# Performance work log

Hardware: AMD Instinct MI355X
Metric: run time of the kernel (lower is better)

The kernel has to match this reference:

```python
import jax, jax.numpy as jnp
import numpy as np

KH, KW = 5, 5               # kernel_size from init_kwargs
PAD_H, PAD_W = (KH - 1) // 2, (KW - 1) // 2
MED_IDX = (KH * KW - 1) // 2  # torch.median -> lower median; exact middle for odd counts


def setup_inputs() -> dict:
    key = jax.random.key(0)
    x = jax.random.normal(key, (2, 4, 1024, 1024), dtype=jnp.float32)  # B,C,H,W
    return {"x": x}


def reference(x):
    # Zero-pad spatially, matching F.conv2d(padding=(k-1)//2), stride=1.
    B, C, H, W = x.shape
    xp = jnp.pad(x, ((0, 0), (0, 0), (PAD_H, PAD_H), (PAD_W, PAD_W)))
    # Extract K*K shifted views (equivalent to the binary grouped conv2d),
    # stacked into [B, C, KH*KW, H, W] — same layout as features.view(b,c,-1,h,w).
    patches = jnp.stack(
        [xp[:, :, i:i + H, j:j + W] for i in range(KH) for j in range(KW)],
        axis=2,
    )
    # torch.median(dim=2)[0]: sort the window axis and take the middle element.
    return jnp.sort(patches, axis=2)[:, :, MED_IDX]
```

## Files before the change

kernel.cpp:

```cpp
#include <hip/hip_runtime.h>

#define IMG_W 1024
#define IMG_H 1024

typedef _Float16 h2 __attribute__((ext_vector_type(2)));

__device__ __forceinline__ h2 mn(h2 a, h2 b) {
    h2 r; asm("v_pk_min_f16 %0, %1, %2" : "=v"(r) : "v"(a), "v"(b)); return r;
}
__device__ __forceinline__ h2 mx(h2 a, h2 b) {
    h2 r; asm("v_pk_max_f16 %0, %1, %2" : "=v"(r) : "v"(a), "v"(b)); return r;
}
__device__ __forceinline__ void ce(h2 &a, h2 &b) { h2 t = mn(a, b); b = mx(a, b); a = t; }
__device__ __forceinline__ h2 med3p(h2 a, h2 b, h2 c) {
    return mx(mn(a, b), mn(mx(a, b), c));
}
__device__ __forceinline__ void sort5(h2 &a0, h2 &a1, h2 &a2, h2 &a3, h2 &a4) {
    ce(a0, a1); ce(a3, a4); ce(a2, a4); ce(a2, a3);
    ce(a0, a3); ce(a0, a2); ce(a1, a4); ce(a1, a3); ce(a1, a2);
}
__device__ __forceinline__ void sort4(h2 &a, h2 &b, h2 &c, h2 &d) {
    ce(a, b); ce(c, d); ce(a, c); ce(b, d); ce(b, c);
}

__device__ __forceinline__ h2 bch2(unsigned u) { return __builtin_bit_cast(h2, u); }

struct Row { h2 a, b, c, d, e; };
struct Raw { unsigned d0, d1, d2; };

#define LDS_DW 35
#define LDS_PAD 2560

__device__ __forceinline__ Raw load_raw(const unsigned* __restrict__ ldsf, int row, int tx) {
    const unsigned* p = ldsf + row * LDS_DW + tx;
    Raw r; r.d0 = p[0]; r.d1 = p[1]; r.d2 = p[2];
    return r;
}
__device__ __forceinline__ Row sort_row(Raw r) {
    h2 p0 = bch2(r.d0);
    h2 p1 = bch2((r.d0 >> 16) | (r.d1 << 16));
    h2 p2 = bch2(r.d1);
    h2 p3 = bch2((r.d1 >> 16) | (r.d2 << 16));
    h2 p4 = bch2(r.d2);
    sort5(p0, p1, p2, p3, p4);
    return {p0, p1, p2, p3, p4};
}

__device__ __forceinline__ h2 tail13(h2 A, h2 B, h2 c1a, h2 c1b, h2 c1c,
                                     h2 c2a, h2 c2b, h2 c2c,
                                     h2 c3a, h2 c3b, h2 c3c, h2 D, h2 E) {
    ce(A, D); ce(c1a, c3a); ce(A, c1a);
    ce(B, E); ce(c1b, c3b); ce(E, c3b);
    h2 e0 = B, e1 = D, e2 = E, e3 = c1a, e4 = c1b, e5 = c3a, e6 = c1c;
    ce(e0, e1); ce(e2, e3); ce(e4, e5);
    ce(e0, e2); ce(e4, e6); ce(e0, e4);
    ce(e1, e3); ce(e5, e6); ce(e3, e6);
    h2 f0 = e1, f1 = e2, f2 = e3, f3 = e4, f4 = e5, f5 = c2a;
    ce(f0, f1); ce(f2, f3); ce(f4, f5);
    ce(f0, f2); ce(f0, f4);
    ce(f1, f3); ce(f3, f5);
    h2 g0 = f1, g1 = f2, g2 = f3, g3 = f4, g4 = c2b;
    ce(g0, g1); ce(g2, g3);
    ce(g0, g2); ce(g0, g4);
    ce(g1, g3); ce(g3, g4);
    h2 h0 = g1, h1 = g2, h2_ = g3, h3 = c2c;
    ce(h0, h1); ce(h2_, h3); ce(h0, h2_); ce(h1, h3);
    return med3p(h1, h2_, c3c);
}

__device__ __forceinline__ void pair_medians(const Row &rb, const Row &rc, const Row &rd,
                                             const Row &re, const Row &ra, const Row &rf,
                                             h2 &out_lo, h2 &out_hi) {
    h2 s0, s1, s2, s3;
    s0 = rb.a; s1 = rc.a; s2 = rd.a; s3 = re.a; sort4(s0, s1, s2, s3);
    h2 Bl = mx(s3, ra.a), Al = mx(s2, mn(s3, ra.a));
    h2 Bh = mx(s3, rf.a), Ah = mx(s2, mn(s3, rf.a));
    s0 = rb.b; s1 = rc.b; s2 = rd.b; s3 = re.b; sort4(s0, s1, s2, s3);
    h2 c1al = s2, c1bl = s3, c1cl = mx(s1, ra.b);
    h2 c1ah = s2, c1bh = s3, c1ch = mx(s1, rf.b);
    s0 = rb.c; s1 = rc.c; s2 = rd.c; s3 = re.c; sort4(s0, s1, s2, s3);
    h2 c2al = s1, c2bl = s2, c2cl = med3p(s0, ra.c, s3);
    h2 c2ah = s1, c2bh = s2, c2ch = med3p(s0, rf.c, s3);
    s0 = rb.d; s1 = rc.d; s2 = rd.d; s3 = re.d; sort4(s0, s1, s2, s3);
    h2 c3al = s0, c3bl = s1, c3cl = mn(s2, ra.d);
    h2 c3ah = s0, c3bh = s1, c3ch = mn(s2, rf.d);
    s0 = rb.e; s1 = rc.e; s2 = rd.e; s3 = re.e; sort4(s0, s1, s2, s3);
    h2 Dl = mn(s0, ra.e), El = mn(s1, mx(s0, ra.e));
    h2 Dh = mn(s0, rf.e), Eh = mn(s1, mx(s0, rf.e));

    out_lo = tail13(Al, Bl, c1al, c1bl, c1cl, c2al, c2bl, c2cl, c3al, c3bl, c3cl, Dl, El);
    out_hi = tail13(Ah, Bh, c1ah, c1bh, c1ch, c2ah, c2bh, c2ch, c3ah, c3bh, c3ch, Dh, Eh);
}

__global__ __launch_bounds__(256, 4) void median5x5_kernel(const float* __restrict__ x,
                                                           float* __restrict__ out) {
    __shared__ unsigned ldsf[LDS_PAD];

    const int tx = threadIdx.x;
    const int ty = threadIdx.y;
    const int tid = ty * 32 + tx;
    const int plane = blockIdx.z;
    const float* src = x + (size_t)plane * IMG_H * IMG_W;

    const int gx0 = blockIdx.x * 64 - 2;
    const int gy0 = blockIdx.y * 64 - 2;

    float2 v[10];
    int oka[10], okb[10];
    #pragma unroll
    for (int k = 0; k < 10; ++k) {
        int idx = tid + k * 256;
        int r = idx / LDS_DW;
        int dc = idx - r * LDS_DW;
        int gy = gy0 + r;
        int gxa = gx0 + 2 * dc;
        int cgy = min(max(gy, 0), IMG_H - 1);
        int cgx = min(max(gxa, 0), IMG_W - 2);
        v[k] = *reinterpret_cast<const float2*>(src + (size_t)cgy * IMG_W + cgx);
        oka[k] = ((unsigned)gy < IMG_H) & ((unsigned)gxa < IMG_W);
        okb[k] = ((unsigned)gy < IMG_H) & ((unsigned)(gxa + 1) < IMG_W);
    }
    #pragma unroll
    for (int k = 0; k < 10; ++k) {
        int idx = tid + k * 256;
        float a = oka[k] ? v[k].x : 0.0f;
        float b = okb[k] ? v[k].y : 0.0f;
        ldsf[idx] = __builtin_bit_cast(unsigned, __builtin_amdgcn_cvt_pkrtz(a, b));
    }
    __syncthreads();

    const int base = ty * 8;
    Raw r0 = load_raw(ldsf, base + 0, tx), r1 = load_raw(ldsf, base + 1, tx),
        r2 = load_raw(ldsf, base + 2, tx), r3 = load_raw(ldsf, base + 3, tx),
        r4 = load_raw(ldsf, base + 4, tx), r5 = load_raw(ldsf, base + 5, tx);
    Row S0 = sort_row(r0), S1 = sort_row(r1), S2 = sort_row(r2),
        S3 = sort_row(r3), S4 = sort_row(r4), S5 = sort_row(r5);

    float* dst = out + (size_t)plane * IMG_H * IMG_W
               + (size_t)(blockIdx.y * 64 + base) * IMG_W + blockIdx.x * 64 + 2 * tx;
    h2 mlo, mhi;

#define EMIT(vv, m) do {                                                       \
        float2 o; o.x = (float)(m).x; o.y = (float)(m).y;                      \
        *reinterpret_cast<float2*>(dst + (size_t)(vv) * IMG_W) = o;            \
    } while (0)

    Raw n0 = load_raw(ldsf, base + 6, tx), n1 = load_raw(ldsf, base + 7, tx);
    pair_medians(S1, S2, S3, S4, S0, S5, mlo, mhi);
    EMIT(0, mlo); EMIT(1, mhi);
    S0 = sort_row(n0); S1 = sort_row(n1);

    n0 = load_raw(ldsf, base + 8, tx); n1 = load_raw(ldsf, base + 9, tx);
    pair_medians(S3, S4, S5, S0, S2, S1, mlo, mhi);
    EMIT(2, mlo); EMIT(3, mhi);
    S2 = sort_row(n0); S3 = sort_row(n1);

    n0 = load_raw(ldsf, base + 10, tx); n1 = load_raw(ldsf, base + 11, tx);
    pair_medians(S5, S0, S1, S2, S4, S3, mlo, mhi);
    EMIT(4, mlo); EMIT(5, mhi);
    S4 = sort_row(n0); S5 = sort_row(n1);

    pair_medians(S1, S2, S3, S4, S0, S5, mlo, mhi);
    EMIT(6, mlo); EMIT(7, mhi);
#undef EMIT
}

extern "C" void kernel_launch(void* const* d_in, const int* in_sizes, int n_in,
                              void* d_out, int out_size, void* d_ws, size_t ws_size,
                              hipStream_t stream) {
    const float* x = (const float*)d_in[0];
    float* out = (float*)d_out;
    const int planes = in_sizes[0] / (IMG_H * IMG_W);
    dim3 grid(IMG_W / 64, IMG_H / 64, planes);
    dim3 block(32, 8);
    median5x5_kernel<<<grid, block, 0, stream>>>(x, out);
}
```

Baseline: 90.30 us.

## Process two vertical tiles per block with double-buffered LDS prefetch

Each block now handles two 64x64 output tiles stacked vertically. The global loads for the second tile are issued before the first tile is computed, so their latency hides behind the sorting work, and the staged data goes into a second LDS buffer. This halves the grid and doubles LDS per block. It also keeps 30 extra registers live across the compute phase, which may lower occupancy or cause spills under the 256x4 launch bounds.

```diff
diff --git a/kernel.cpp b/kernel.cpp
--- a/kernel.cpp
+++ b/kernel.cpp
@@ -92,21 +92,13 @@
     out_hi = tail13(Ah, Bh, c1ah, c1bh, c1ch, c2ah, c2bh, c2ch, c3ah, c3bh, c3ch, Dh, Eh);
 }
 
-__global__ __launch_bounds__(256, 4) void median5x5_kernel(const float* __restrict__ x,
-                                                           float* __restrict__ out) {
-    __shared__ unsigned ldsf[LDS_PAD];
-
-    const int tx = threadIdx.x;
-    const int ty = threadIdx.y;
-    const int tid = ty * 32 + tx;
-    const int plane = blockIdx.z;
-    const float* src = x + (size_t)plane * IMG_H * IMG_W;
-
-    const int gx0 = blockIdx.x * 64 - 2;
-    const int gy0 = blockIdx.y * 64 - 2;
-
+struct Stage {
     float2 v[10];
     int oka[10], okb[10];
+};
+
+__device__ __forceinline__ void stage_issue(const float* __restrict__ src,
+                                            int gx0, int gy0, int tid, Stage &st) {
     #pragma unroll
     for (int k = 0; k < 10; ++k) {
         int idx = tid + k * 256;
@@ -116,28 +108,30 @@
         int gxa = gx0 + 2 * dc;
         int cgy = min(max(gy, 0), IMG_H - 1);
         int cgx = min(max(gxa, 0), IMG_W - 2);
-        v[k] = *reinterpret_cast<const float2*>(src + (size_t)cgy * IMG_W + cgx);
-        oka[k] = ((unsigned)gy < IMG_H) & ((unsigned)gxa < IMG_W);
-        okb[k] = ((unsigned)gy < IMG_H) & ((unsigned)(gxa + 1) < IMG_W);
+        st.v[k] = *reinterpret_cast<const float2*>(src + (size_t)cgy * IMG_W + cgx);
+        st.oka[k] = ((unsigned)gy < IMG_H) & ((unsigned)gxa < IMG_W);
+        st.okb[k] = ((unsigned)gy < IMG_H) & ((unsigned)(gxa + 1) < IMG_W);
     }
+}
+
+__device__ __forceinline__ void stage_write(unsigned* __restrict__ buf,
+                                            int tid, const Stage &st) {
     #pragma unroll
     for (int k = 0; k < 10; ++k) {
         int idx = tid + k * 256;
-        float a = oka[k] ? v[k].x : 0.0f;
-        float b = okb[k] ? v[k].y : 0.0f;
-        ldsf[idx] = __builtin_bit_cast(unsigned, __builtin_amdgcn_cvt_pkrtz(a, b));
+        float a = st.oka[k] ? st.v[k].x : 0.0f;
+        float b = st.okb[k] ? st.v[k].y : 0.0f;
+        buf[idx] = __builtin_bit_cast(unsigned, __builtin_amdgcn_cvt_pkrtz(a, b));
     }
-    __syncthreads();
-
-    const int base = ty * 8;
+}
+
+__device__ __forceinline__ void compute_tile(const unsigned* __restrict__ ldsf,
+                                             int base, int tx, float* __restrict__ dst) {
     Raw r0 = load_raw(ldsf, base + 0, tx), r1 = load_raw(ldsf, base + 1, tx),
         r2 = load_raw(ldsf, base + 2, tx), r3 = load_raw(ldsf, base + 3, tx),
         r4 = load_raw(ldsf, base + 4, tx), r5 = load_raw(ldsf, base + 5, tx);
     Row S0 = sort_row(r0), S1 = sort_row(r1), S2 = sort_row(r2),
         S3 = sort_row(r3), S4 = sort_row(r4), S5 = sort_row(r5);
-
-    float* dst = out + (size_t)plane * IMG_H * IMG_W
-               + (size_t)(blockIdx.y * 64 + base) * IMG_W + blockIdx.x * 64 + 2 * tx;
     h2 mlo, mhi;
 
 #define EMIT(vv, m) do {                                                       \
@@ -163,6 +157,35 @@
     pair_medians(S1, S2, S3, S4, S0, S5, mlo, mhi);
     EMIT(6, mlo); EMIT(7, mhi);
 #undef EMIT
+}
+
+__global__ __launch_bounds__(256, 4) void median5x5_kernel(const float* __restrict__ x,
+                                                           float* __restrict__ out) {
+    __shared__ unsigned ldsf[2][LDS_PAD];
+
+    const int tx = threadIdx.x;
+    const int ty = threadIdx.y;
+    const int tid = ty * 32 + tx;
+    const int plane = blockIdx.z;
+    const float* src = x + (size_t)plane * IMG_H * IMG_W;
+
+    const int gx0 = blockIdx.x * 64 - 2;
+    const int ty0 = blockIdx.y * 128;
+    const int base = ty * 8;
+
+    float* dst0 = out + (size_t)plane * IMG_H * IMG_W
+                + (size_t)(ty0 + base) * IMG_W + blockIdx.x * 64 + 2 * tx;
+    float* dst1 = dst0 + (size_t)64 * IMG_W;
+
+    Stage s0, s1;
+    stage_issue(src, gx0, ty0 - 2, tid, s0);
+    stage_write(ldsf[0], tid, s0);
+    __syncthreads();
+    stage_issue(src, gx0, ty0 + 62, tid, s1);
+    compute_tile(ldsf[0], base, tx, dst0);
+    stage_write(ldsf[1], tid, s1);
+    __syncthreads();
+    compute_tile(ldsf[1], base, tx, dst1);
 }
 
 extern "C" void kernel_launch(void* const* d_in, const int* in_sizes, int n_in,
@@ -171,7 +194,7 @@
     const float* x = (const float*)d_in[0];
     float* out = (float*)d_out;
     const int planes = in_sizes[0] / (IMG_H * IMG_W);
-    dim3 grid(IMG_W / 64, IMG_H / 64, planes);
+    dim3 grid(IMG_W / 64, IMG_H / 128, planes);
     dim3 block(32, 8);
     median5x5_kernel<<<grid, block, 0, stream>>>(x, out);
 }
```

Measured after the change: 90.67 us. About the same (+0.4%).

## Load interior tiles directly into LDS as fp32 via global_load_lds

Applied to the files above, without the earlier changes.

Interior blocks now copy their 68x72 fp32 halo tile straight from global memory into LDS with 16-byte global_load_lds, bypassing registers. The fp16 packing moves to read time, converting each window pair with cvt_pkrtz. Border blocks keep a clamped, zero-padded float2 path. The LDS tile doubles in size because it is stored as fp32, the occupancy hint rises to 6, and the inline-asm min/max become builtins. The aim is fewer VGPRs and instructions in the staging phase, at the cost of more LDS traffic and extra conversions in the compute loop.

```diff
diff --git a/kernel.cpp b/kernel.cpp
--- a/kernel.cpp
+++ b/kernel.cpp
@@ -2,18 +2,21 @@
 
 #define IMG_W 1024
 #define IMG_H 1024
+#define ROW_F 72
+#define LDS_F 5120
 
 typedef _Float16 h2 __attribute__((ext_vector_type(2)));
+typedef __attribute__((address_space(3))) unsigned lds_u32_t;
+typedef const __attribute__((address_space(1))) unsigned glb_u32_t;
 
-__device__ __forceinline__ h2 mn(h2 a, h2 b) {
-    h2 r; asm("v_pk_min_f16 %0, %1, %2" : "=v"(r) : "v"(a), "v"(b)); return r;
-}
-__device__ __forceinline__ h2 mx(h2 a, h2 b) {
-    h2 r; asm("v_pk_max_f16 %0, %1, %2" : "=v"(r) : "v"(a), "v"(b)); return r;
-}
+__device__ __forceinline__ h2 mn(h2 a, h2 b) { return __builtin_elementwise_min(a, b); }
+__device__ __forceinline__ h2 mx(h2 a, h2 b) { return __builtin_elementwise_max(a, b); }
 __device__ __forceinline__ void ce(h2 &a, h2 &b) { h2 t = mn(a, b); b = mx(a, b); a = t; }
 __device__ __forceinline__ h2 med3p(h2 a, h2 b, h2 c) {
     return mx(mn(a, b), mn(mx(a, b), c));
+}
+__device__ __forceinline__ h2 pkrtz(float a, float b) {
+    return __builtin_bit_cast(h2, __builtin_amdgcn_cvt_pkrtz(a, b));
 }
 __device__ __forceinline__ void sort5(h2 &a0, h2 &a1, h2 &a2, h2 &a3, h2 &a4) {
     ce(a0, a1); ce(a3, a4); ce(a2, a4); ce(a2, a3);
@@ -23,25 +26,23 @@
     ce(a, b); ce(c, d); ce(a, c); ce(b, d); ce(b, c);
 }
 
-__device__ __forceinline__ h2 bch2(unsigned u) { return __builtin_bit_cast(h2, u); }
+struct Row { h2 a, b, c, d, e; };
+struct Raw { float2 f01, f23, f45; };
 
-struct Row { h2 a, b, c, d, e; };
-struct Raw { unsigned d0, d1, d2; };
-
-#define LDS_DW 35
-#define LDS_PAD 2560
-
-__device__ __forceinline__ Raw load_raw(const unsigned* __restrict__ ldsf, int row, int tx) {
-    const unsigned* p = ldsf + row * LDS_DW + tx;
-    Raw r; r.d0 = p[0]; r.d1 = p[1]; r.d2 = p[2];
+__device__ __forceinline__ Raw load_raw(const float* __restrict__ ldsf, int row, int tx) {
+    const float* p = ldsf + row * ROW_F + 2 * tx + 2;
+    Raw r;
+    r.f01 = *reinterpret_cast<const float2*>(p);
+    r.f23 = *reinterpret_cast<const float2*>(p + 2);
+    r.f45 = *reinterpret_cast<const float2*>(p + 4);
     return r;
 }
 __device__ __forceinline__ Row sort_row(Raw r) {
-    h2 p0 = bch2(r.d0);
-    h2 p1 = bch2((r.d0 >> 16) | (r.d1 << 16));
-    h2 p2 = bch2(r.d1);
-    h2 p3 = bch2((r.d1 >> 16) | (r.d2 << 16));
-    h2 p4 = bch2(r.d2);
+    h2 p0 = pkrtz(r.f01.x, r.f01.y);
+    h2 p1 = pkrtz(r.f01.y, r.f23.x);
+    h2 p2 = pkrtz(r.f23.x, r.f23.y);
+    h2 p3 = pkrtz(r.f23.y, r.f45.x);
+    h2 p4 = pkrtz(r.f45.x, r.f45.y);
     sort5(p0, p1, p2, p3, p4);
     return {p0, p1, p2, p3, p4};
 }
@@ -92,40 +93,52 @@
     out_hi = tail13(Ah, Bh, c1ah, c1bh, c1ch, c2ah, c2bh, c2ch, c3ah, c3bh, c3ch, Dh, Eh);
 }
 
-__global__ __launch_bounds__(256, 4) void median5x5_kernel(const float* __restrict__ x,
+__global__ __launch_bounds__(256, 6) void median5x5_kernel(const float* __restrict__ x,
                                                            float* __restrict__ out) {
-    __shared__ unsigned ldsf[LDS_PAD];
+    __shared__ float ldsf[LDS_F];
 
     const int tx = threadIdx.x;
     const int ty = threadIdx.y;
     const int tid = ty * 32 + tx;
+    const int bx = blockIdx.x, by = blockIdx.y;
     const int plane = blockIdx.z;
     const float* src = x + (size_t)plane * IMG_H * IMG_W;
 
-    const int gx0 = blockIdx.x * 64 - 2;
-    const int gy0 = blockIdx.y * 64 - 2;
+    const int gx0a = bx * 64 - 4;
+    const int gy0 = by * 64 - 2;
 
-    float2 v[10];
-    int oka[10], okb[10];
-    #pragma unroll
-    for (int k = 0; k < 10; ++k) {
-        int idx = tid + k * 256;
-        int r = idx / LDS_DW;
-        int dc = idx - r * LDS_DW;
-        int gy = gy0 + r;
-        int gxa = gx0 + 2 * dc;
-        int cgy = min(max(gy, 0), IMG_H - 1);
-        int cgx = min(max(gxa, 0), IMG_W - 2);
-        v[k] = *reinterpret_cast<const float2*>(src + (size_t)cgy * IMG_W + cgx);
-        oka[k] = ((unsigned)gy < IMG_H) & ((unsigned)gxa < IMG_W);
-        okb[k] = ((unsigned)gy < IMG_H) & ((unsigned)(gxa + 1) < IMG_W);
-    }
-    #pragma unroll
-    for (int k = 0; k < 10; ++k) {
-        int idx = tid + k * 256;
-        float a = oka[k] ? v[k].x : 0.0f;
-        float b = okb[k] ? v[k].y : 0.0f;
-        ldsf[idx] = __builtin_bit_cast(unsigned, __builtin_amdgcn_cvt_pkrtz(a, b));
+    const bool border = (bx == 0) | (bx == 15) | (by == 0) | (by == 15);
+    if (!border) {
+        const float* srcb = src + (size_t)gy0 * IMG_W + gx0a;
+        #pragma unroll
+        for (int k = 0; k < 5; ++k) {
+            int q = k * 256 + tid;
+            int row = q / 18;
+            int c4 = q - row * 18;
+            const float* g = srcb + row * IMG_W + c4 * 4;
+            __builtin_amdgcn_global_load_lds((glb_u32_t*)g, (lds_u32_t*)&ldsf[q * 4],
+                                             16, 0, 0);
+        }
+        asm volatile("s_waitcnt vmcnt(0)" ::: "memory");
+    } else {
+        #pragma unroll
+        for (int k = 0; k < 10; ++k) {
+            int idx = tid + k * 256;
+            if (idx < 68 * 36) {
+                int r = idx / 36;
+                int dc = idx - r * 36;
+                int gy = gy0 + r;
+                int gxa = gx0a + 2 * dc;
+                int cgy = min(max(gy, 0), IMG_H - 1);
+                int cgx = min(max(gxa, 0), IMG_W - 2);
+                float2 v = *reinterpret_cast<const float2*>(src + (size_t)cgy * IMG_W + cgx);
+                bool rowok = (unsigned)gy < (unsigned)IMG_H;
+                float a = (rowok && (unsigned)gxa < (unsigned)IMG_W) ? v.x : 0.0f;
+                float b = (rowok && (unsigned)(gxa + 1) < (unsigned)IMG_W) ? v.y : 0.0f;
+                float2 w2; w2.x = a; w2.y = b;
+                *reinterpret_cast<float2*>(&ldsf[r * ROW_F + 2 * dc]) = w2;
+            }
+        }
     }
     __syncthreads();
 
@@ -137,7 +150,7 @@
         S3 = sort_row(r3), S4 = sort_row(r4), S5 = sort_row(r5);
 
     float* dst = out + (size_t)plane * IMG_H * IMG_W
-               + (size_t)(blockIdx.y * 64 + base) * IMG_W + blockIdx.x * 64 + 2 * tx;
+               + (size_t)(by * 64 + base) * IMG_W + bx * 64 + 2 * tx;
     h2 mlo, mhi;
 
 #define EMIT(vv, m) do {                                                       \
```

After: 94.61 us. 1.05x slower.
